# Optimization experiments

Measured on AMD Instinct MI355X. Metric: run time of the kernel, lower is better.

## Reference

```python
import jax, jax.numpy as jnp
import numpy as np

SIGMAS = [0.5, 1.0, 2.0, 4.0, 8.0]
DATA_RANGE = 1.0
C1 = (0.01 * DATA_RANGE) ** 2
C2 = (0.03 * DATA_RANGE) ** 2
ALPHA = 0.025
COMPENSATION = 200.0
PAD = int(2 * SIGMAS[-1])            # 16
FILTER_SIZE = int(4 * SIGMAS[-1] + 1)  # 33


def _gauss_2d(size: int, sigma: float) -> np.ndarray:
    coords = np.arange(size, dtype=np.float32) - size // 2
    g = np.exp(-coords ** 2 / (2.0 * sigma ** 2))
    g /= g.sum()
    return np.outer(g, g)


def _make_g_masks() -> jnp.ndarray:
    # (3 * n_sigmas, 1, F, F): three identical masks per sigma, as in the torch buffer
    masks = np.zeros((3 * len(SIGMAS), 1, FILTER_SIZE, FILTER_SIZE), dtype=np.float32)
    for idx, sigma in enumerate(SIGMAS):
        k = _gauss_2d(FILTER_SIZE, sigma)
        masks[3 * idx + 0, 0] = k
        masks[3 * idx + 1, 0] = k
        masks[3 * idx + 2, 0] = k
    return jnp.asarray(masks)


def _gconv(x: jnp.ndarray, w: jnp.ndarray, groups: int) -> jnp.ndarray:
    return jax.lax.conv_general_dilated(
        x, w, window_strides=(1, 1), padding=[(PAD, PAD), (PAD, PAD)],
        dimension_numbers=("NCHW", "OIHW", "NCHW"), feature_group_count=groups)


def setup_inputs() -> dict:
    key = jax.random.key(0)
    k1, k2 = jax.random.split(key)
    img1 = jax.random.uniform(k1, (8, 3, 512, 512), dtype=jnp.float32)
    img2 = jax.random.uniform(k2, (8, 3, 512, 512), dtype=jnp.float32)
    return {"img1": img1, "img2": img2}


def reference(img1, img2):
    g_masks = _make_g_masks()
    ch = img1.shape[1]

    mux = _gconv(img1, g_masks, ch)           # (B, 15, H, W)
    muy = _gconv(img2, g_masks, ch)
    mux2 = mux * mux
    muy2 = muy * muy
    muxy = mux * muy
    sigmax2 = _gconv(img1 * img1, g_masks, ch) - mux2
    sigmay2 = _gconv(img2 * img2, g_masks, ch) - muy2
    sigmaxy = _gconv(img1 * img2, g_masks, ch) - muxy

    lc = (2.0 * muxy + C1) / (mux2 + muy2 + C1)
    cs = (2.0 * sigmaxy + C2) / (sigmax2 + sigmay2 + C2)

    lM = lc[:, -1] * lc[:, -2] * lc[:, -3]    # (B, H, W)
    PIcs = jnp.prod(cs, axis=1)               # (B, H, W)
    loss_ms_ssim = 1.0 - lM * PIcs

    loss_l1 = jnp.abs(img1 - img2)
    gaussian_l1 = _gconv(loss_l1, g_masks[-ch:], ch).mean(axis=1)  # (B, H, W)

    loss = ALPHA * loss_ms_ssim + (1.0 - ALPHA) * gaussian_l1 / DATA_RANGE
    return (COMPENSATION * loss).mean()
```

## Files before the change

### kernel.cpp

```cpp
#include <hip/hip_runtime.h>
#include <math.h>

struct GW { float w[171]; };
constexpr int W05 = 0;
constexpr int W1  = 21;
constexpr int W2  = 46;
constexpr int W4  = 81;
constexpr int W8  = 122;

namespace {

constexpr float kC1 = 1e-4f;
constexpr float kC2 = 9e-4f;


template<int R, int WOFF>
__device__ __forceinline__ void hpass4(const GW& g, const float* __restrict__ sS,
                                       const float* __restrict__ sD,
                                       float4* __restrict__ hb, int t) {
  constexpr int NROWS = 32 + 2 * R;
  constexpr int NE = NROWS * 8;
  constexpr int QS = (16 - R) & ~3;
  constexpr int NG = ((19 + R - QS) >> 2) + 1;
  if (t >= NE) return;
  const int hrow = t >> 3;
  const int cg = t & 7;
  const int srow = hrow + (16 - R);
  const int rx = srow & 7;
  const int rowbase = srow << 6;
  const int g0 = cg + (QS >> 2);
  float a0[4] = {0.f, 0.f, 0.f, 0.f}, a1[4] = {0.f, 0.f, 0.f, 0.f};
  float a2[4] = {0.f, 0.f, 0.f, 0.f}, a3[4] = {0.f, 0.f, 0.f, 0.f};
#pragma unroll 2
  for (int j = 0; j < NG; ++j) {
    const int off = rowbase + (((g0 + j) ^ rx) << 2);
    const int wb = WOFF + 8 + QS - 16 + R + 4 * j;
    const float4 s4 = *reinterpret_cast<const float4*>(&sS[off]);
    const float4 d4 = *reinterpret_cast<const float4*>(&sD[off]);
    const float* sp = reinterpret_cast<const float*>(&s4);
    const float* dp = reinterpret_cast<const float*>(&d4);
#pragma unroll
    for (int u = 0; u < 4; ++u) {
      const float sv = sp[u], dv = dp[u];
      const float s2 = sv * sv, d2 = dv * dv;
#pragma unroll
      for (int o = 0; o < 4; ++o) {
        const float wk = g.w[wb + u - o];
        a0[o] += wk * sv; a1[o] += wk * dv;
        a2[o] += wk * s2; a3[o] += wk * d2;
      }
    }
  }
  const int rb = hrow << 5;
#pragma unroll
  for (int o = 0; o < 4; ++o) {
    const int c = (cg << 2) + o;
    hb[rb + (c ^ ((c >> 3) & 3))] = make_float4(a0[o], a1[o], a2[o], a3[o]);
  }
}

template<int R, int WOFF>
__device__ __forceinline__ void vpass4(const GW& g, const float4* __restrict__ hb,
                                       int vc, int vr0,
                                       float (&o0)[2], float (&o1)[2],
                                       float (&o2)[2], float (&o3)[2]) {
#pragma unroll
  for (int i = 0; i < 2; ++i) { o0[i] = o1[i] = o2[i] = o3[i] = 0.f; }
  const int fc = vc ^ ((vc >> 3) & 3);
#pragma unroll 2
  for (int jj = 0; jj < 2 * R + 2; ++jj) {
    const float4 v = hb[((vr0 + jj) << 5) + fc];
    const int wb = WOFF + 8 + jj;
#pragma unroll
    for (int i = 0; i < 2; ++i) {
      const float wk = g.w[wb - i];
      o0[i] += wk * v.x; o1[i] += wk * v.y;
      o2[i] += wk * v.z; o3[i] += wk * v.w;
    }
  }
}

template<int R, int WOFF, int MULT, bool DOLM>
__device__ __forceinline__ void sweep4(const GW& g,
    const float* sS, const float* sD, float4* hb, int t, int vc, int vr0,
    float (&PI)[2], float (&lM)[2]) {
  __syncthreads();
  hpass4<R, WOFF>(g, sS, sD, hb, t);
  __syncthreads();
  float os[2], od[2], os2[2], od2[2];
  vpass4<R, WOFF>(g, hb, vc, vr0, os, od, os2, od2);
#pragma unroll
  for (int i = 0; i < 2; ++i) {
    const float vs = os2[i] - os[i] * os[i];
    const float vd = od2[i] - od[i] * od[i];
    const float cs = (0.5f * (vs - vd) + kC2) / (0.5f * (vs + vd) + kC2);
    float p = cs;
    if constexpr (MULT > 1) p *= cs;
    if constexpr (MULT > 2) p *= cs;
    PI[i] *= p;
    if constexpr (DOLM) {
      const float sa = os[i] * os[i], sb = od[i] * od[i];
      const float lc = (0.5f * (sa - sb) + kC1) / (0.5f * (sa + sb) + kC1);
      lM[i] = lc * lc * lc;
    }
  }
}

template<int R, int WOFF>
__device__ __forceinline__ void hpassL1(const GW& g, const float* __restrict__ sD,
                                        float* __restrict__ hbl, int t) {
  constexpr int QS = (16 - R) & ~3;
  constexpr int NG = ((19 + R - QS) >> 2) + 1;
  const int hrow = t >> 3;
  const int cg = t & 7;
  const int rx = hrow & 7;
  const int rowbase = hrow << 6;
  const int g0 = cg + (QS >> 2);
  float a0[4] = {0.f, 0.f, 0.f, 0.f};
#pragma unroll 2
  for (int j = 0; j < NG; ++j) {
    const int off = rowbase + (((g0 + j) ^ rx) << 2);
    const int wb = WOFF + 8 + QS - 16 + R + 4 * j;
    const float4 d4 = *reinterpret_cast<const float4*>(&sD[off]);
    const float* dp = reinterpret_cast<const float*>(&d4);
#pragma unroll
    for (int u = 0; u < 4; ++u) {
      const float av = dp[u];
#pragma unroll
      for (int o = 0; o < 4; ++o) a0[o] += g.w[wb + u - o] * av;
    }
  }
  *reinterpret_cast<float4*>(&hbl[(hrow << 5) + (cg << 2)]) =
      make_float4(a0[0], a0[1], a0[2], a0[3]);
}

template<int R, int WOFF>
__device__ __forceinline__ void sweepL1_fused(const GW& g, float* sD, float* hbl,
                                              const float (&al1)[8], int t,
                                              int vc, int vr0, float (&l1s)[2]) {
#pragma unroll
  for (int e = 0; e < 2; ++e) {
    const int gidx = t + (e << 9);
    const int ly = gidx >> 4, lg = gidx & 15;
    const int off = (ly << 6) + ((lg ^ (ly & 7)) << 2);
    *reinterpret_cast<float4*>(&sD[off]) =
        make_float4(al1[4 * e], al1[4 * e + 1], al1[4 * e + 2], al1[4 * e + 3]);
  }
  __syncthreads();
  hpassL1<R, WOFF>(g, sD, hbl, t);
  __syncthreads();
#pragma unroll 2
  for (int jj = 0; jj < 2 * R + 2; ++jj) {
    const float vl = hbl[((vr0 + jj) << 5) + vc];
    const int wb = WOFF + 8 + jj;
#pragma unroll
    for (int i = 0; i < 2; ++i) l1s[i] += g.w[wb - i] * vl;
  }
}

__device__ __forceinline__ void load_tile(const float* __restrict__ p1,
                                          const float* __restrict__ p2,
                                          float* __restrict__ sS, float* __restrict__ sD,
                                          float (&al1)[8], int t, int gx0, int gy0) {
#pragma unroll 1
  for (int e = 0; e < 2; ++e) {
    const int gidx = t + (e << 9);
    const int ly = gidx >> 4, lg = gidx & 15;
    const int gy = gy0 + ly;
    const int gx = gx0 + (lg << 2);
    float4 a = make_float4(0.f, 0.f, 0.f, 0.f);
    float4 b = make_float4(0.f, 0.f, 0.f, 0.f);
    if (gy >= 0 && gy < 512) {
      if (gx >= 0 && gx + 3 < 512) {
        a = *reinterpret_cast<const float4*>(&p1[(gy << 9) + gx]);
        b = *reinterpret_cast<const float4*>(&p2[(gy << 9) + gx]);
      } else {
        float* ap = reinterpret_cast<float*>(&a);
        float* bp = reinterpret_cast<float*>(&b);
#pragma unroll
        for (int u = 0; u < 4; ++u) {
          const int x = gx + u;
          if (x >= 0 && x < 512) { ap[u] = p1[(gy << 9) + x]; bp[u] = p2[(gy << 9) + x]; }
        }
      }
    }
    float4 s, d;
    s.x = a.x + b.x; s.y = a.y + b.y; s.z = a.z + b.z; s.w = a.w + b.w;
    d.x = a.x - b.x; d.y = a.y - b.y; d.z = a.z - b.z; d.w = a.w - b.w;
    al1[4 * e + 0] += fabsf(d.x); al1[4 * e + 1] += fabsf(d.y);
    al1[4 * e + 2] += fabsf(d.z); al1[4 * e + 3] += fabsf(d.w);
    const int off = (ly << 6) + ((lg ^ (ly & 7)) << 2);
    *reinterpret_cast<float4*>(&sS[off]) = s;
    *reinterpret_cast<float4*>(&sD[off]) = d;
  }
}

}

extern "C" __global__ __launch_bounds__(512) void msssim_main(
    const float* __restrict__ img1, const float* __restrict__ img2,
    float* __restrict__ partial, GW g) {
  __shared__ __align__(16) float sS[4096];
  __shared__ __align__(16) float sD[4096];
  __shared__ __align__(16) float4 hb[2048];
  __shared__ float red[8];
  float* hbl = reinterpret_cast<float*>(hb);

  const int t = threadIdx.x;

  const int bid = (int)blockIdx.x + ((int)blockIdx.y << 4) + ((int)blockIdx.z << 8);
  const int swz = ((bid & 7) << 8) + (bid >> 3);
  const int bx = swz & 15, by = (swz >> 4) & 15, b = swz >> 8;

  const int gx0 = bx * 32 - 16;
  const int gy0 = by * 32 - 16;
  const int vc = t & 31;
  const int vr0 = (t >> 5) << 1;

  float PI[2] = {1.f, 1.f};
  float lM[2] = {0.f, 0.f};
  float l1s[2] = {0.f, 0.f};
  float al1[8] = {0.f, 0.f, 0.f, 0.f, 0.f, 0.f, 0.f, 0.f};

  {
    const float* p1 = img1 + (((size_t)b * 3 + 0) << 18);
    const float* p2 = img2 + (((size_t)b * 3 + 0) << 18);
    load_tile(p1, p2, sS, sD, al1, t, gx0, gy0);
    sweep4<2, W05, 3, false>(g, sS, sD, hb, t, vc, vr0, PI, lM);
    sweep4<4, W1, 2, false>(g, sS, sD, hb, t, vc, vr0, PI, lM);
  }
  {
    const float* p1 = img1 + (((size_t)b * 3 + 1) << 18);
    const float* p2 = img2 + (((size_t)b * 3 + 1) << 18);
    load_tile(p1, p2, sS, sD, al1, t, gx0, gy0);
    sweep4<4, W1, 1, false>(g, sS, sD, hb, t, vc, vr0, PI, lM);
    sweep4<9, W2, 3, false>(g, sS, sD, hb, t, vc, vr0, PI, lM);
    sweep4<12, W4, 1, false>(g, sS, sD, hb, t, vc, vr0, PI, lM);
  }
  {
    const float* p1 = img1 + (((size_t)b * 3 + 2) << 18);
    const float* p2 = img2 + (((size_t)b * 3 + 2) << 18);
    load_tile(p1, p2, sS, sD, al1, t, gx0, gy0);
    sweep4<12, W4, 2, false>(g, sS, sD, hb, t, vc, vr0, PI, lM);
    sweep4<16, W8, 3, true>(g, sS, sD, hb, t, vc, vr0, PI, lM);
  }
  sweepL1_fused<16, W8>(g, sD, hbl, al1, t, vc, vr0, l1s);

  float s = 0.f;
#pragma unroll
  for (int i = 0; i < 2; ++i)
    s += 0.025f * (1.f - lM[i] * PI[i]) + 0.975f * (l1s[i] * (1.f / 3.f));

#pragma unroll
  for (int off = 32; off >= 1; off >>= 1) s += __shfl_down(s, off, 64);
  if ((t & 63) == 0) red[t >> 6] = s;
  __syncthreads();
  if (t == 0) {
    float tot = 0.f;
#pragma unroll
    for (int i = 0; i < 8; ++i) tot += red[i];
    partial[swz] = tot;
  }
}

extern "C" __global__ __launch_bounds__(256) void msssim_reduce(
    const float* __restrict__ partial, float* __restrict__ out, int n) {
  __shared__ float red[4];
  float s = 0.f;
  for (int i = threadIdx.x; i < n; i += 256) s += partial[i];
#pragma unroll
  for (int off = 32; off >= 1; off >>= 1) s += __shfl_down(s, off, 64);
  if ((threadIdx.x & 63) == 0) red[threadIdx.x >> 6] = s;
  __syncthreads();
  if (threadIdx.x == 0) {
    out[0] = (red[0] + red[1] + red[2] + red[3]) * (200.0f / 2097152.0f);
  }
}

extern "C" void kernel_launch(void* const* d_in, const int* in_sizes, int n_in,
                              void* d_out, int out_size, void* d_ws, size_t ws_size,
                              hipStream_t stream) {
  const float* img1 = (const float*)d_in[0];
  const float* img2 = (const float*)d_in[1];
  float* out = (float*)d_out;
  float* partial = (float*)d_ws;

  GW g;
  {
    const double sig[5] = {0.5, 1.0, 2.0, 4.0, 8.0};
    const int R[5] = {2, 4, 9, 12, 16};
    const int off[5] = {W05, W1, W2, W4, W8};
    for (int i = 0; i < 5; ++i) {
      double tmp[17];
      double sum = 0.0;
      for (int k = 0; k <= R[i]; ++k) {
        tmp[k] = exp(-(double)(k * k) / (2.0 * sig[i] * sig[i]));
        sum += (k ? 2.0 : 1.0) * tmp[k];
      }
      const int len = 2 * R[i] + 17;
      for (int m = 0; m < len; ++m) {
        int d = m - 8 - R[i];
        if (d < 0) d = -d;
        g.w[off[i] + m] = (m >= 8 && m <= 8 + 2 * R[i]) ? (float)(tmp[d] / sum) : 0.0f;
      }
    }
  }

  dim3 grid(16, 16, 8);
  msssim_main<<<grid, dim3(512), 0, stream>>>(img1, img2, partial, g);
  msssim_reduce<<<1, dim3(256), 0, stream>>>(partial, out, 2048);
}
```

Before: 128.9 us.

## Split vertical pass across wavefront halves with 4-row register blocking and shuffle combine

Vertical Gaussian pass now has each thread compute partial sums for 4 output rows over half the window taps. The two halves of a 64-lane wavefront cover the upper and lower taps and are combined with a cross-half shuffle. Each LDS row loaded is reused for 4 outputs instead of 2, which cuts LDS reads per output and moves weights into registers. The cost is more registers per thread and extra shuffle instructions, which could lower occupancy.

```diff
diff --git a/kernel.cpp b/kernel.cpp
--- a/kernel.cpp
+++ b/kernel.cpp
@@ -60,35 +60,54 @@
 }
 
 template<int R, int WOFF>
-__device__ __forceinline__ void vpass4(const GW& g, const float4* __restrict__ hb,
-                                       int vc, int vr0,
-                                       float (&o0)[2], float (&o1)[2],
-                                       float (&o2)[2], float (&o3)[2]) {
-#pragma unroll
-  for (int i = 0; i < 2; ++i) { o0[i] = o1[i] = o2[i] = o3[i] = 0.f; }
-  const int fc = vc ^ ((vc >> 3) & 3);
-#pragma unroll 2
-  for (int jj = 0; jj < 2 * R + 2; ++jj) {
-    const float4 v = hb[((vr0 + jj) << 5) + fc];
-    const int wb = WOFF + 8 + jj;
-#pragma unroll
-    for (int i = 0; i < 2; ++i) {
-      const float wk = g.w[wb - i];
+__device__ __forceinline__ void vpass_part(const GW& g, const float4* __restrict__ hb,
+                                           int fc, int vr0, int half,
+                                           float (&o0)[4], float (&o1)[4],
+                                           float (&o2)[4], float (&o3)[4]) {
+#pragma unroll
+  for (int i = 0; i < 4; ++i) { o0[i] = o1[i] = o2[i] = o3[i] = 0.f; }
+  float W[R + 5];
+#pragma unroll
+  for (int m = 0; m < R + 5; ++m)
+    W[m] = half ? g.w[WOFF + 7 + R + m] : g.w[WOFF + 5 + m];
+  const float4* __restrict__ hbp =
+      hb + ((vr0 + (half ? (R + 2) : 0)) << 5) + fc;
+#pragma unroll
+  for (int k = 0; k < R + 2; ++k) {
+    const float4 v = hbp[k << 5];
+#pragma unroll
+    for (int i = 0; i < 4; ++i) {
+      const float wk = W[k - i + 3];
       o0[i] += wk * v.x; o1[i] += wk * v.y;
       o2[i] += wk * v.z; o3[i] += wk * v.w;
     }
   }
 }
 
+__device__ __forceinline__ void combine2(int half, const float (&o)[4],
+                                         float (&keep)[2]) {
+#pragma unroll
+  for (int j = 0; j < 2; ++j) {
+    const float send = half ? o[j] : o[j + 2];
+    const float recv = __shfl_xor(send, 32, 64);
+    keep[j] = (half ? o[j + 2] : o[j]) + recv;
+  }
+}
+
 template<int R, int WOFF, int MULT, bool DOLM>
 __device__ __forceinline__ void sweep4(const GW& g,
-    const float* sS, const float* sD, float4* hb, int t, int vc, int vr0,
-    float (&PI)[2], float (&lM)[2]) {
+    const float* sS, const float* sD, float4* hb, int t, int fc, int vr0,
+    int half, float (&PI)[2], float (&lM)[2]) {
   __syncthreads();
   hpass4<R, WOFF>(g, sS, sD, hb, t);
   __syncthreads();
+  float p0[4], p1[4], p2[4], p3[4];
+  vpass_part<R, WOFF>(g, hb, fc, vr0, half, p0, p1, p2, p3);
   float os[2], od[2], os2[2], od2[2];
-  vpass4<R, WOFF>(g, hb, vc, vr0, os, od, os2, od2);
+  combine2(half, p0, os);
+  combine2(half, p1, od);
+  combine2(half, p2, os2);
+  combine2(half, p3, od2);
 #pragma unroll
   for (int i = 0; i < 2; ++i) {
     const float vs = os2[i] - os[i] * os[i];
@@ -137,7 +156,8 @@
 template<int R, int WOFF>
 __device__ __forceinline__ void sweepL1_fused(const GW& g, float* sD, float* hbl,
                                               const float (&al1)[8], int t,
-                                              int vc, int vr0, float (&l1s)[2]) {
+                                              int vc, int vr0, int half,
+                                              float (&l1s)[2]) {
 #pragma unroll
   for (int e = 0; e < 2; ++e) {
     const int gidx = t + (e << 9);
@@ -149,13 +169,23 @@
   __syncthreads();
   hpassL1<R, WOFF>(g, sD, hbl, t);
   __syncthreads();
-#pragma unroll 2
-  for (int jj = 0; jj < 2 * R + 2; ++jj) {
-    const float vl = hbl[((vr0 + jj) << 5) + vc];
-    const int wb = WOFF + 8 + jj;
-#pragma unroll
-    for (int i = 0; i < 2; ++i) l1s[i] += g.w[wb - i] * vl;
-  }
+  float W[R + 5];
+#pragma unroll
+  for (int m = 0; m < R + 5; ++m)
+    W[m] = half ? g.w[WOFF + 7 + R + m] : g.w[WOFF + 5 + m];
+  float lp[4] = {0.f, 0.f, 0.f, 0.f};
+  const float* __restrict__ hblp =
+      hbl + ((vr0 + (half ? (R + 2) : 0)) << 5) + vc;
+#pragma unroll
+  for (int k = 0; k < R + 2; ++k) {
+    const float vl = hblp[k << 5];
+#pragma unroll
+    for (int i = 0; i < 4; ++i) lp[i] += W[k - i + 3] * vl;
+  }
+  float keep[2];
+  combine2(half, lp, keep);
+#pragma unroll
+  for (int j = 0; j < 2; ++j) l1s[j] += keep[j];
 }
 
 __device__ __forceinline__ void load_tile(const float* __restrict__ p1,
@@ -215,7 +245,9 @@
   const int gx0 = bx * 32 - 16;
   const int gy0 = by * 32 - 16;
   const int vc = t & 31;
-  const int vr0 = (t >> 5) << 1;
+  const int half = (t >> 5) & 1;
+  const int vr0 = (t >> 6) << 2;
+  const int fc = vc ^ ((vc >> 3) & 3);
 
   float PI[2] = {1.f, 1.f};
   float lM[2] = {0.f, 0.f};
@@ -226,25 +258,25 @@
     const float* p1 = img1 + (((size_t)b * 3 + 0) << 18);
     const float* p2 = img2 + (((size_t)b * 3 + 0) << 18);
     load_tile(p1, p2, sS, sD, al1, t, gx0, gy0);
-    sweep4<2, W05, 3, false>(g, sS, sD, hb, t, vc, vr0, PI, lM);
-    sweep4<4, W1, 2, false>(g, sS, sD, hb, t, vc, vr0, PI, lM);
+    sweep4<2, W05, 3, false>(g, sS, sD, hb, t, fc, vr0, half, PI, lM);
+    sweep4<4, W1, 2, false>(g, sS, sD, hb, t, fc, vr0, half, PI, lM);
   }
   {
     const float* p1 = img1 + (((size_t)b * 3 + 1) << 18);
     const float* p2 = img2 + (((size_t)b * 3 + 1) << 18);
     load_tile(p1, p2, sS, sD, al1, t, gx0, gy0);
-    sweep4<4, W1, 1, false>(g, sS, sD, hb, t, vc, vr0, PI, lM);
-    sweep4<9, W2, 3, false>(g, sS, sD, hb, t, vc, vr0, PI, lM);
-    sweep4<12, W4, 1, false>(g, sS, sD, hb, t, vc, vr0, PI, lM);
+    sweep4<4, W1, 1, false>(g, sS, sD, hb, t, fc, vr0, half, PI, lM);
+    sweep4<9, W2, 3, false>(g, sS, sD, hb, t, fc, vr0, half, PI, lM);
+    sweep4<12, W4, 1, false>(g, sS, sD, hb, t, fc, vr0, half, PI, lM);
   }
   {
     const float* p1 = img1 + (((size_t)b * 3 + 2) << 18);
     const float* p2 = img2 + (((size_t)b * 3 + 2) << 18);
     load_tile(p1, p2, sS, sD, al1, t, gx0, gy0);
-    sweep4<12, W4, 2, false>(g, sS, sD, hb, t, vc, vr0, PI, lM);
-    sweep4<16, W8, 3, true>(g, sS, sD, hb, t, vc, vr0, PI, lM);
-  }
-  sweepL1_fused<16, W8>(g, sD, hbl, al1, t, vc, vr0, l1s);
+    sweep4<12, W4, 2, false>(g, sS, sD, hb, t, fc, vr0, half, PI, lM);
+    sweep4<16, W8, 3, true>(g, sS, sD, hb, t, fc, vr0, half, PI, lM);
+  }
+  sweepL1_fused<16, W8>(g, sD, hbl, al1, t, vc, vr0, half, l1s);
 
   float s = 0.f;
 #pragma unroll
```

New measurement: 192.8 us. 49.6% more time.
